# Performance work log

Hardware: AMD Instinct MI355X
Metric: run time of the kernel (lower is better)

The kernel has to match this reference:

```python
import jax, jax.numpy as jnp
import numpy as np

B, S, D = 2, 2048, 1024
E, K, F = 8, 2, 4 * D


def setup_inputs() -> dict:
    key = jax.random.key(0)
    ks = jax.random.split(key, 5)
    sd = 1.0 / np.sqrt(D)
    sf = 1.0 / np.sqrt(F)
    x = jax.random.normal(ks[0], (B, S, D), dtype=jnp.float32)
    Wg = jax.random.uniform(ks[1], (D, E), dtype=jnp.float32, minval=-sd, maxval=sd)
    W1 = jax.random.uniform(ks[2], (E, D, F), dtype=jnp.float32, minval=-sd, maxval=sd)
    W3 = jax.random.uniform(ks[3], (D, E * F), dtype=jnp.float32, minval=-sd, maxval=sd).reshape(D, E, F).transpose(1, 0, 2)
    W2 = jax.random.uniform(ks[4], (E, F, D), dtype=jnp.float32, minval=-sf, maxval=sf)
    return {"x": x, "Wg": Wg, "W1": W1, "W2": W2, "W3": W3}


def reference(x, Wg, W1, W2, W3):
    Bx, Sx, Dx = x.shape
    xf = x.reshape(-1, Dx)  # [T, D]
    T = xf.shape[0]
    gate_logits = xf @ Wg  # [T, E]
    probs = jax.nn.softmax(gate_logits, axis=-1)
    weights, sel = jax.lax.top_k(probs, K)  # [T, K]
    weights = weights / jnp.sum(weights, axis=-1, keepdims=True)
    # scatter top-k weights into a dense [T, E] combine matrix (top-k indices are distinct)
    coef = jnp.zeros((T, W1.shape[0]), dtype=xf.dtype)
    coef = coef.at[jnp.arange(T)[:, None], sel].add(weights)
    out = jnp.zeros_like(xf)
    for e in range(W1.shape[0]):  # small fixed expert count
        h = jax.nn.silu(xf @ W1[e]) * (xf @ W3[e])  # [T, F]
        out = out + coef[:, e:e + 1] * (h @ W2[e])
    aux_loss = jnp.mean(jnp.var(gate_logits, axis=-1, ddof=1))  # torch .var() is unbiased
    return out.reshape(Bx, Sx, Dx), aux_loss
```

## Files before the change

kernel.cpp:

```cpp
#include <hip/hip_runtime.h>

typedef __bf16 bf16x8 __attribute__((ext_vector_type(8)));
typedef float  f32x4  __attribute__((ext_vector_type(4)));

#define TOKS 4096
#define DIM  1024
#define NEXP 8
#define NF   4096
#define CAP  4096
#define BM 128
#define BN 128
#define BK 64

typedef __attribute__((address_space(3))) unsigned int as3_u32;
typedef __attribute__((address_space(1))) unsigned int as1_u32;
__device__ __forceinline__ void gl16(const unsigned short* g, unsigned short* l) {
  __builtin_amdgcn_global_load_lds((as1_u32*)(unsigned long long)g, (as3_u32*)l, 16, 0, 0);
}

__device__ __forceinline__ unsigned short f2bf(float f) {
  unsigned int u = __float_as_uint(f);
  u += 0x7FFFu + ((u >> 16) & 1u);
  return (unsigned short)(u >> 16);
}
__device__ __forceinline__ int swzo(int major) {
  return ((major & 7) ^ ((major >> 3) & 7)) << 3;
}
__device__ __forceinline__ int swz8(int row, int chunk) {
  return (chunk ^ (row & 7)) << 3;
}

__global__ void moe_route(const float* __restrict__ x, const float* __restrict__ Wg,
                          int* __restrict__ pairCnt, int* __restrict__ pairIdx,
                          float* __restrict__ pairWgt, float* __restrict__ auxSum)
{
  int lane = threadIdx.x & 63;
  int tok  = blockIdx.x * 4 + (threadIdx.x >> 6);
  const float* xr = x + (size_t)tok * DIM;
  float acc[8];
  #pragma unroll
  for (int e = 0; e < 8; ++e) acc[e] = 0.f;
  #pragma unroll
  for (int i = 0; i < 16; ++i) {
    int d = i * 64 + lane;
    float xv = xr[d];
    const float4* wr = (const float4*)(Wg + d * 8);
    float4 wa = wr[0], wb = wr[1];
    acc[0] += xv * wa.x; acc[1] += xv * wa.y; acc[2] += xv * wa.z; acc[3] += xv * wa.w;
    acc[4] += xv * wb.x; acc[5] += xv * wb.y; acc[6] += xv * wb.z; acc[7] += xv * wb.w;
  }
  #pragma unroll
  for (int e = 0; e < 8; ++e) {
    float v = acc[e];
    #pragma unroll
    for (int off = 32; off; off >>= 1) v += __shfl_xor(v, off);
    acc[e] = v;
  }
  if (lane == 0) {
    int e1 = 0; float l1 = acc[0];
    #pragma unroll
    for (int e = 1; e < 8; ++e) if (acc[e] > l1) { l1 = acc[e]; e1 = e; }
    int e2 = -1; float l2 = -3.4e38f;
    #pragma unroll
    for (int e = 0; e < 8; ++e) if (e != e1 && acc[e] > l2) { l2 = acc[e]; e2 = e; }
    float r  = expf(l2 - l1);
    float w1 = 1.f / (1.f + r);
    float w2 = r / (1.f + r);
    int s1 = atomicAdd(&pairCnt[e1], 1);
    pairIdx[e1 * CAP + s1] = tok * 2;     pairWgt[e1 * CAP + s1] = w1;
    int s2 = atomicAdd(&pairCnt[e2], 1);
    pairIdx[e2 * CAP + s2] = tok * 2 + 1; pairWgt[e2 * CAP + s2] = w2;
    float m = 0.f;
    #pragma unroll
    for (int e = 0; e < 8; ++e) m += acc[e];
    m *= 0.125f;
    float v = 0.f;
    #pragma unroll
    for (int e = 0; e < 8; ++e) { float dd = acc[e] - m; v += dd * dd; }
    atomicAdd(auxSum, v * (1.f / 7.f));
  }
}

__global__ void moe_aux_final(const float* __restrict__ auxSum, float* __restrict__ outScalar) {
  *outScalar = auxSum[0] * (1.f / (float)TOKS);
}

__global__ __launch_bounds__(256) void cvt_x(const float* __restrict__ in,
                                             unsigned short* __restrict__ o)
{
  int i = (blockIdx.x * 256 + threadIdx.x) * 16;
  const float4* s = (const float4*)(in + i);
  float4 a = s[0], b = s[1], c = s[2], d = s[3];
  union { unsigned short u[8]; uint4 q; } p0, p1;
  p0.u[0]=f2bf(a.x); p0.u[1]=f2bf(a.y); p0.u[2]=f2bf(a.z); p0.u[3]=f2bf(a.w);
  p0.u[4]=f2bf(b.x); p0.u[5]=f2bf(b.y); p0.u[6]=f2bf(b.z); p0.u[7]=f2bf(b.w);
  p1.u[0]=f2bf(c.x); p1.u[1]=f2bf(c.y); p1.u[2]=f2bf(c.z); p1.u[3]=f2bf(c.w);
  p1.u[4]=f2bf(d.x); p1.u[5]=f2bf(d.y); p1.u[6]=f2bf(d.z); p1.u[7]=f2bf(d.w);
  *(uint4*)(o + i)     = p0.q;
  *(uint4*)(o + i + 8) = p1.q;
}

__global__ __launch_bounds__(256) void cvt_transpose(
    const float* __restrict__ in, unsigned short* __restrict__ outp, int R, int C)
{
  __shared__ unsigned short tile[64 * 72];
  int e  = blockIdx.z;
  int r0 = blockIdx.x * 64, c0 = blockIdx.y * 64;
  const float*    ine  = in   + (size_t)e * R * C;
  unsigned short* oute = outp + (size_t)e * R * C;
  int t = threadIdx.x;
  int r = t >> 2, cs = (t & 3) * 16;
  const float4* src = (const float4*)(ine + (size_t)(r0 + r) * C + c0 + cs);
  #pragma unroll
  for (int j = 0; j < 4; ++j) {
    float4 v = src[j];
    tile[(cs + j * 4 + 0) * 72 + r] = f2bf(v.x);
    tile[(cs + j * 4 + 1) * 72 + r] = f2bf(v.y);
    tile[(cs + j * 4 + 2) * 72 + r] = f2bf(v.z);
    tile[(cs + j * 4 + 3) * 72 + r] = f2bf(v.w);
  }
  __syncthreads();
  int c = t >> 2, rs = (t & 3) * 16;
  uint4 o0 = *(const uint4*)&tile[c * 72 + rs];
  uint4 o1 = *(const uint4*)&tile[c * 72 + rs + 8];
  unsigned short* dst = oute + (size_t)(c0 + c) * R + r0 + rs;
  *(uint4*)dst       = o0;
  *(uint4*)(dst + 8) = o1;
}

__global__ __launch_bounds__(256) void cvt_w13(
    const float* __restrict__ W1, const float* __restrict__ W3,
    unsigned short* __restrict__ outp)
{
  __shared__ unsigned short t1[64 * 72];
  __shared__ unsigned short t3[64 * 72];
  int e  = blockIdx.z;
  int r0 = blockIdx.x * 64, c0 = blockIdx.y * 64;
  const float* in1 = W1 + (size_t)e * DIM * NF;
  const float* in3 = W3 + (size_t)e * DIM * NF;
  unsigned short* oute = outp + (size_t)e * (2 * NF) * DIM;
  int t = threadIdx.x;
  int r = t >> 2, cs = (t & 3) * 16;
  const float4* s1 = (const float4*)(in1 + (size_t)(r0 + r) * NF + c0 + cs);
  const float4* s3 = (const float4*)(in3 + (size_t)(r0 + r) * NF + c0 + cs);
  #pragma unroll
  for (int j = 0; j < 4; ++j) {
    float4 v1 = s1[j];
    float4 v3 = s3[j];
    int cb = cs + j * 4;
    t1[(cb + 0) * 72 + r] = f2bf(v1.x);
    t1[(cb + 1) * 72 + r] = f2bf(v1.y);
    t1[(cb + 2) * 72 + r] = f2bf(v1.z);
    t1[(cb + 3) * 72 + r] = f2bf(v1.w);
    t3[(cb + 0) * 72 + r] = f2bf(v3.x);
    t3[(cb + 1) * 72 + r] = f2bf(v3.y);
    t3[(cb + 2) * 72 + r] = f2bf(v3.z);
    t3[(cb + 3) * 72 + r] = f2bf(v3.w);
  }
  __syncthreads();
  int c = t >> 2, rs = (t & 3) * 16;
  int drow = c0 * 2 + (c >> 4) * 32 + (c & 15);
  uint4 a0 = *(const uint4*)&t1[c * 72 + rs];
  uint4 a1 = *(const uint4*)&t1[c * 72 + rs + 8];
  uint4 b0 = *(const uint4*)&t3[c * 72 + rs];
  uint4 b1 = *(const uint4*)&t3[c * 72 + rs + 8];
  unsigned short* d1 = oute + (size_t)drow * DIM + r0 + rs;
  unsigned short* d3 = d1 + (size_t)16 * DIM;
  *(uint4*)d1       = a0;
  *(uint4*)(d1 + 8) = a1;
  *(uint4*)d3       = b0;
  *(uint4*)(d3 + 8) = b1;
}

#define FFN1_PHASE(CUR, NXT, KS, Q, STG, DOWAIT, KTN) do {                       \
  int kc_ = (KS) * 4 + (lane >> 4);                                              \
  int sz_ = ((kc_ ^ (lane & 7)) << 3);                                           \
  int ar_ = wr * 128 + (Q) * 64 + (lane & 15);                                   \
  int br_ = wc * 64 + (lane & 15);                                               \
  bf16x8 a0_ = *(const bf16x8*)&As_[CUR][(ar_     ) * 64 + sz_];                 \
  bf16x8 a1_ = *(const bf16x8*)&As_[CUR][(ar_ + 16) * 64 + sz_];                 \
  bf16x8 a2_ = *(const bf16x8*)&As_[CUR][(ar_ + 32) * 64 + sz_];                 \
  bf16x8 a3_ = *(const bf16x8*)&As_[CUR][(ar_ + 48) * 64 + sz_];                 \
  bf16x8 b0_ = *(const bf16x8*)&Bs_[CUR][(br_     ) * 64 + sz_];                 \
  bf16x8 b1_ = *(const bf16x8*)&Bs_[CUR][(br_ + 16) * 64 + sz_];                 \
  bf16x8 b2_ = *(const bf16x8*)&Bs_[CUR][(br_ + 32) * 64 + sz_];                 \
  bf16x8 b3_ = *(const bf16x8*)&Bs_[CUR][(br_ + 48) * 64 + sz_];                 \
  if ((STG) == 1) {                                                              \
    gl16(pA[0][0] + (KTN), &As_[NXT][(w * 16      ) * 64]);                      \
    gl16(pA[0][1] + (KTN), &As_[NXT][(w * 16 +   8) * 64]);                      \
    gl16(pA[1][0] + (KTN), &As_[NXT][(w * 16 + 128) * 64]);                      \
    gl16(pA[1][1] + (KTN), &As_[NXT][(w * 16 + 136) * 64]);                      \
  } else if ((STG) == 2) {                                                       \
    gl16(pB[0][0] + (KTN), &Bs_[NXT][(w * 16      ) * 64]);                      \
    gl16(pB[0][1] + (KTN), &Bs_[NXT][(w * 16 +   8) * 64]);                      \
    gl16(pB[1][0] + (KTN), &Bs_[NXT][(w * 16 + 128) * 64]);                      \
    gl16(pB[1][1] + (KTN), &Bs_[NXT][(w * 16 + 136) * 64]);                      \
  }                                                                              \
  if (DOWAIT) {                                                                  \
    asm volatile("s_waitcnt lgkmcnt(0)" ::: "memory");                           \
    asm volatile("s_waitcnt vmcnt(0)" ::: "memory");                             \
  }                                                                              \
  __builtin_amdgcn_s_barrier();                                                  \
  __builtin_amdgcn_s_setprio(1);                                                 \
  acc[(Q)*4+0][0] = __builtin_amdgcn_mfma_f32_16x16x32_bf16(a0_, b0_, acc[(Q)*4+0][0], 0,0,0); \
  acc[(Q)*4+1][0] = __builtin_amdgcn_mfma_f32_16x16x32_bf16(a1_, b0_, acc[(Q)*4+1][0], 0,0,0); \
  acc[(Q)*4+2][0] = __builtin_amdgcn_mfma_f32_16x16x32_bf16(a2_, b0_, acc[(Q)*4+2][0], 0,0,0); \
  acc[(Q)*4+3][0] = __builtin_amdgcn_mfma_f32_16x16x32_bf16(a3_, b0_, acc[(Q)*4+3][0], 0,0,0); \
  acc[(Q)*4+0][1] = __builtin_amdgcn_mfma_f32_16x16x32_bf16(a0_, b1_, acc[(Q)*4+0][1], 0,0,0); \
  acc[(Q)*4+1][1] = __builtin_amdgcn_mfma_f32_16x16x32_bf16(a1_, b1_, acc[(Q)*4+1][1], 0,0,0); \
  acc[(Q)*4+2][1] = __builtin_amdgcn_mfma_f32_16x16x32_bf16(a2_, b1_, acc[(Q)*4+2][1], 0,0,0); \
  acc[(Q)*4+3][1] = __builtin_amdgcn_mfma_f32_16x16x32_bf16(a3_, b1_, acc[(Q)*4+3][1], 0,0,0); \
  acc[(Q)*4+0][2] = __builtin_amdgcn_mfma_f32_16x16x32_bf16(a0_, b2_, acc[(Q)*4+0][2], 0,0,0); \
  acc[(Q)*4+1][2] = __builtin_amdgcn_mfma_f32_16x16x32_bf16(a1_, b2_, acc[(Q)*4+1][2], 0,0,0); \
  acc[(Q)*4+2][2] = __builtin_amdgcn_mfma_f32_16x16x32_bf16(a2_, b2_, acc[(Q)*4+2][2], 0,0,0); \
  acc[(Q)*4+3][2] = __builtin_amdgcn_mfma_f32_16x16x32_bf16(a3_, b2_, acc[(Q)*4+3][2], 0,0,0); \
  acc[(Q)*4+0][3] = __builtin_amdgcn_mfma_f32_16x16x32_bf16(a0_, b3_, acc[(Q)*4+0][3], 0,0,0); \
  acc[(Q)*4+1][3] = __builtin_amdgcn_mfma_f32_16x16x32_bf16(a1_, b3_, acc[(Q)*4+1][3], 0,0,0); \
  acc[(Q)*4+2][3] = __builtin_amdgcn_mfma_f32_16x16x32_bf16(a2_, b3_, acc[(Q)*4+2][3], 0,0,0); \
  acc[(Q)*4+3][3] = __builtin_amdgcn_mfma_f32_16x16x32_bf16(a3_, b3_, acc[(Q)*4+3][3], 0,0,0); \
  __builtin_amdgcn_s_setprio(0);                                                 \
} while (0)

#define FFN1_GROUP(CUR, NXT, KTN)           \
  FFN1_PHASE(CUR, NXT, 0, 0, 1, 0, KTN);    \
  FFN1_PHASE(CUR, NXT, 0, 1, 2, 0, KTN);    \
  FFN1_PHASE(CUR, NXT, 1, 0, 0, 0, KTN);    \
  FFN1_PHASE(CUR, NXT, 1, 1, 0, 1, KTN);

__global__ __launch_bounds__(512, 2) void moe_ffn1_8p(
    const unsigned short* __restrict__ xbf, const unsigned short* __restrict__ W13T,
    const int* __restrict__ pairCnt, const int* __restrict__ pairIdx,
    unsigned short* __restrict__ hbuf)
{
  int bid = blockIdx.x;
  int n_t = (bid & 7) | (((bid >> 7) & 3) << 3);
  int m_t = (bid >> 3) & 15;
  int e   = bid >> 9;
  int cnt = pairCnt[e];
  int m0  = m_t * 256;
  if (m0 >= cnt) return;
  __shared__ __attribute__((aligned(16))) unsigned short As_[2][256 * 64];
  __shared__ __attribute__((aligned(16))) unsigned short Bs_[2][256 * 64];
  __shared__ int rowPid[256];
  int tid = threadIdx.x, lane = tid & 63, w = tid >> 6;
  if (tid < 256) {
    int gi = m0 + tid;
    rowPid[tid] = (gi < cnt) ? pairIdx[e * CAP + gi] : -1;
  }
  const unsigned short* W13e = W13T + (size_t)e * (2 * NF) * DIM + (size_t)n_t * 256 * DIM;
  int wr = w >> 2, wc = w & 3;
  f32x4 zero = {0.f, 0.f, 0.f, 0.f};
  f32x4 acc[8][4];
  #pragma unroll
  for (int mi = 0; mi < 8; ++mi)
    #pragma unroll
    for (int ni = 0; ni < 4; ++ni) acc[mi][ni] = zero;
  __syncthreads();

  int sr = w * 16 + (lane >> 3);
  int sc = ((lane & 7) ^ (lane >> 3)) * 8;
  const unsigned short* pA[2][2];
  const unsigned short* pB[2][2];
  #pragma unroll
  for (int h = 0; h < 2; ++h) {
    #pragma unroll
    for (int k = 0; k < 2; ++k) {
      int R = h * 128 + sr + k * 8;
      int pid = rowPid[R];
      pA[h][k] = xbf + (size_t)((pid >= 0) ? (pid >> 1) : 0) * DIM + sc;
      pB[h][k] = W13e + (size_t)R * DIM + sc;
    }
  }
  gl16(pA[0][0], &As_[0][(w * 16      ) * 64]);
  gl16(pA[0][1], &As_[0][(w * 16 +   8) * 64]);
  gl16(pA[1][0], &As_[0][(w * 16 + 128) * 64]);
  gl16(pA[1][1], &As_[0][(w * 16 + 136) * 64]);
  gl16(pB[0][0], &Bs_[0][(w * 16      ) * 64]);
  gl16(pB[0][1], &Bs_[0][(w * 16 +   8) * 64]);
  gl16(pB[1][0], &Bs_[0][(w * 16 + 128) * 64]);
  gl16(pB[1][1], &Bs_[0][(w * 16 + 136) * 64]);
  asm volatile("s_waitcnt vmcnt(0)" ::: "memory");
  __builtin_amdgcn_s_barrier();

  for (int j = 0; j < 16; j += 2) {
    int ktn0 = (j + 1) * 64;
    int ktn1 = (j + 2 < 16) ? (j + 2) * 64 : (j + 1) * 64;
    FFN1_GROUP(0, 1, ktn0);
    FFN1_GROUP(1, 0, ktn1);
  }

  #pragma unroll
  for (int mi = 0; mi < 8; ++mi) {
    #pragma unroll
    for (int r = 0; r < 4; ++r) {
      int row = wr * 128 + mi * 16 + ((lane >> 4) << 2) + r;
      int pid = rowPid[row];
      if (pid < 0) continue;
      size_t hb = (size_t)pid * NF + n_t * 128 + wc * 32 + (lane & 15);
      #pragma unroll
      for (int fg = 0; fg < 2; ++fg) {
        float a = acc[mi][fg * 2 + 0][r];
        float g = acc[mi][fg * 2 + 1][r];
        float s = 1.f / (1.f + __expf(-a));
        hbuf[hb + fg * 16] = f2bf(a * s * g);
      }
    }
  }
}

__global__ __launch_bounds__(512) void moe_ffn2_g(
    const unsigned short* __restrict__ hbuf, const unsigned short* __restrict__ W2T,
    const int* __restrict__ pairCnt, const int* __restrict__ pairIdx,
    const float* __restrict__ pairWgt, float* __restrict__ out)
{
  int bid = blockIdx.x;
  int n_t = bid & 7;
  int m_t = (bid >> 3) & 31;
  int e   = bid >> 8;
  int cnt = pairCnt[e];
  int m0  = m_t * BM;
  if (m0 >= cnt) return;
  int n0  = n_t * BN;
  __shared__ __attribute__((aligned(16))) unsigned short As[BM * BK];
  __shared__ __attribute__((aligned(16))) unsigned short Bs[BN * BK];
  __shared__ int   rowPid[BM];
  __shared__ float rowW[BM];
  int tid = threadIdx.x, lane = tid & 63, wid = tid >> 6;
  if (tid < BM) {
    int gi = m0 + tid;
    if (gi < cnt) { rowPid[tid] = pairIdx[e * CAP + gi]; rowW[tid] = pairWgt[e * CAP + gi]; }
    else          { rowPid[tid] = -1;                    rowW[tid] = 0.f; }
  }
  const unsigned short* W2e = W2T + (size_t)e * DIM * NF + (size_t)n0 * NF;
  f32x4 zero = {0.f, 0.f, 0.f, 0.f};
  f32x4 acc[2][4];
  #pragma unroll
  for (int mi = 0; mi < 2; ++mi)
    #pragma unroll
    for (int ni = 0; ni < 4; ++ni) acc[mi][ni] = zero;
  int wm = (wid >> 1) * 32, wn = (wid & 1) * 64;
  __syncthreads();

  int r0a = wid * 16 + (lane >> 3), r1a = r0a + 8;
  int p0 = rowPid[r0a], p1 = rowPid[r1a];
  size_t h0 = (size_t)((p0 >= 0) ? p0 : 0);
  size_t h1 = (size_t)((p1 >= 0) ? p1 : 0);
  int ch0 = ((lane & 7) ^ (r0a & 7)) * 8;
  int ch1 = ((lane & 7) ^ (r1a & 7)) * 8;
  const unsigned short* gA0 = hbuf + h0 * NF + ch0;
  const unsigned short* gA1 = hbuf + h1 * NF + ch1;
  const unsigned short* gB0 = W2e + (size_t)r0a * NF + ch0;
  const unsigned short* gB1 = W2e + (size_t)r1a * NF + ch1;
  unsigned short* lA0 = &As[(wid * 16) * BK];
  unsigned short* lA1 = &As[(wid * 16 + 8) * BK];
  unsigned short* lB0 = &Bs[(wid * 16) * BK];
  unsigned short* lB1 = &Bs[(wid * 16 + 8) * BK];

  for (int kt = 0; kt < NF; kt += BK) {
    gl16(gA0 + kt, lA0); gl16(gA1 + kt, lA1);
    gl16(gB0 + kt, lB0); gl16(gB1 + kt, lB1);
    __syncthreads();
    #pragma unroll
    for (int ks = 0; ks < 2; ++ks) {
      int kc = ks * 4 + (lane >> 4);
      bf16x8 af[2];
      #pragma unroll
      for (int mi = 0; mi < 2; ++mi) {
        int row = wm + mi * 16 + (lane & 15);
        af[mi] = *(const bf16x8*)(&As[row * BK + swz8(row, kc)]);
      }
      #pragma unroll
      for (int ni = 0; ni < 4; ++ni) {
        int dc = wn + ni * 16 + (lane & 15);
        bf16x8 b = *(const bf16x8*)(&Bs[dc * BK + swz8(dc, kc)]);
        #pragma unroll
        for (int mi = 0; mi < 2; ++mi)
          acc[mi][ni] = __builtin_amdgcn_mfma_f32_16x16x32_bf16(af[mi], b, acc[mi][ni], 0, 0, 0);
      }
    }
    __syncthreads();
  }
  #pragma unroll
  for (int mi = 0; mi < 2; ++mi) {
    #pragma unroll
    for (int r = 0; r < 4; ++r) {
      int row = wm + mi * 16 + ((lane >> 4) << 2) + r;
      int pid = rowPid[row];
      if (pid < 0) continue;
      float w = rowW[row];
      float* op = out + (size_t)(pid >> 1) * DIM + n0 + wn + (lane & 15);
      #pragma unroll
      for (int ni = 0; ni < 4; ++ni)
        atomicAdd(op + ni * 16, w * acc[mi][ni][r]);
    }
  }
}

__global__ __launch_bounds__(512) void moe_ffn1(
    const float* __restrict__ x, const float* __restrict__ W1, const float* __restrict__ W3,
    const int* __restrict__ pairCnt, const int* __restrict__ pairIdx,
    unsigned short* __restrict__ hbuf)
{
  int e   = blockIdx.z;
  int cnt = pairCnt[e];
  int m0  = blockIdx.x * BM;
  if (m0 >= cnt) return;
  int n0  = blockIdx.y * BN;
  __shared__ __attribute__((aligned(16))) unsigned short As[BM * BK];
  __shared__ __attribute__((aligned(16))) unsigned short B1s[BN * BK];
  __shared__ __attribute__((aligned(16))) unsigned short B3s[BN * BK];
  __shared__ int rowPid[BM];
  int tid = threadIdx.x;
  if (tid < BM) {
    int gi = m0 + tid;
    rowPid[tid] = (gi < cnt) ? pairIdx[e * CAP + gi] : -1;
  }
  const float* W1e = W1 + (size_t)e * DIM * NF;
  const float* W3e = W3 + (size_t)e * DIM * NF;
  f32x4 zero = {0.f, 0.f, 0.f, 0.f};
  f32x4 acc1[2][4], acc2[2][4];
  #pragma unroll
  for (int mi = 0; mi < 2; ++mi)
    #pragma unroll
    for (int ni = 0; ni < 4; ++ni) { acc1[mi][ni] = zero; acc2[mi][ni] = zero; }
  int lane = tid & 63, wid = tid >> 6;
  int wm = (wid >> 1) * 32, wn = (wid & 1) * 64;

  for (int kt = 0; kt < DIM; kt += BK) {
    __syncthreads();
    #pragma unroll
    for (int it = 0; it < 4; ++it) {
      int row = it * 32 + (tid >> 4);
      int dq  = tid & 15;
      int pid = rowPid[row];
      int tk  = (pid >= 0) ? (pid >> 1) : 0;
      float4 v = *(const float4*)(x + (size_t)tk * DIM + kt + dq * 4);
      ushort4 b; b.x = f2bf(v.x); b.y = f2bf(v.y); b.z = f2bf(v.z); b.w = f2bf(v.w);
      *(ushort4*)(&As[row * BK + ((dq * 4) ^ swzo(row))]) = b;
    }
    #pragma unroll
    for (int it = 0; it < 4; ++it) {
      int d  = it * 16 + (tid >> 5);
      int fq = tid & 31;
      size_t go = (size_t)(kt + d) * NF + n0 + fq * 4;
      float4 v1 = *(const float4*)(W1e + go);
      float4 v3 = *(const float4*)(W3e + go);
      const float* p1 = (const float*)&v1;
      const float* p3 = (const float*)&v3;
      #pragma unroll
      for (int i = 0; i < 4; ++i) {
        int f   = fq * 4 + i;
        int idx = f * BK + (d ^ swzo(f));
        B1s[idx] = f2bf(p1[i]);
        B3s[idx] = f2bf(p3[i]);
      }
    }
    __syncthreads();
    #pragma unroll
    for (int ks = 0; ks < 2; ++ks) {
      int kb = ks * 32 + ((lane >> 4) << 3);
      bf16x8 af[2];
      #pragma unroll
      for (int mi = 0; mi < 2; ++mi) {
        int row = wm + mi * 16 + (lane & 15);
        af[mi] = *(const bf16x8*)(&As[row * BK + (kb ^ swzo(row))]);
      }
      #pragma unroll
      for (int ni = 0; ni < 4; ++ni) {
        int f = wn + ni * 16 + (lane & 15);
        bf16x8 b1 = *(const bf16x8*)(&B1s[f * BK + (kb ^ swzo(f))]);
        bf16x8 b3 = *(const bf16x8*)(&B3s[f * BK + (kb ^ swzo(f))]);
        #pragma unroll
        for (int mi = 0; mi < 2; ++mi) {
          acc1[mi][ni] = __builtin_amdgcn_mfma_f32_16x16x32_bf16(af[mi], b1, acc1[mi][ni], 0, 0, 0);
          acc2[mi][ni] = __builtin_amdgcn_mfma_f32_16x16x32_bf16(af[mi], b3, acc2[mi][ni], 0, 0, 0);
        }
      }
    }
  }
  #pragma unroll
  for (int mi = 0; mi < 2; ++mi) {
    #pragma unroll
    for (int r = 0; r < 4; ++r) {
      int row = wm + mi * 16 + ((lane >> 4) << 2) + r;
      int pid = rowPid[row];
      if (pid < 0) continue;
      size_t hb = (size_t)pid * NF + n0 + wn + (lane & 15);
      #pragma unroll
      for (int ni = 0; ni < 4; ++ni) {
        float a = acc1[mi][ni][r];
        float g = acc2[mi][ni][r];
        float s = 1.f / (1.f + __expf(-a));
        hbuf[hb + ni * 16] = f2bf(a * s * g);
      }
    }
  }
}

__global__ __launch_bounds__(512) void moe_ffn2(
    const unsigned short* __restrict__ hbuf, const float* __restrict__ W2,
    const int* __restrict__ pairCnt, const int* __restrict__ pairIdx,
    const float* __restrict__ pairWgt, float* __restrict__ out)
{
  int e   = blockIdx.z;
  int cnt = pairCnt[e];
  int m0  = blockIdx.x * BM;
  if (m0 >= cnt) return;
  int n0  = blockIdx.y * BN;
  __shared__ __attribute__((aligned(16))) unsigned short As[BM * BK];
  __shared__ __attribute__((aligned(16))) unsigned short Bs[BN * BK];
  __shared__ int   rowPid[BM];
  __shared__ float rowW[BM];
  int tid = threadIdx.x;
  if (tid < BM) {
    int gi = m0 + tid;
    if (gi < cnt) { rowPid[tid] = pairIdx[e * CAP + gi]; rowW[tid] = pairWgt[e * CAP + gi]; }
    else          { rowPid[tid] = -1;                    rowW[tid] = 0.f; }
  }
  const float* W2e = W2 + (size_t)e * NF * DIM;
  f32x4 zero = {0.f, 0.f, 0.f, 0.f};
  f32x4 acc[2][4];
  #pragma unroll
  for (int mi = 0; mi < 2; ++mi)
    #pragma unroll
    for (int ni = 0; ni < 4; ++ni) acc[mi][ni] = zero;
  int lane = tid & 63, wid = tid >> 6;
  int wm = (wid >> 1) * 32, wn = (wid & 1) * 64;

  for (int kt = 0; kt < NF; kt += BK) {
    __syncthreads();
    #pragma unroll
    for (int it = 0; it < 2; ++it) {
      int row = it * 64 + (tid >> 3);
      int c8  = tid & 7;
      int pid = rowPid[row];
      int pr  = (pid >= 0) ? pid : 0;
      uint4 v = *(const uint4*)(hbuf + (size_t)pr * NF + kt + c8 * 8);
      *(uint4*)(&As[row * BK + ((c8 * 8) ^ swzo(row))]) = v;
    }
    #pragma unroll
    for (int it = 0; it < 4; ++it) {
      int fk = it * 16 + (tid >> 5);
      int dq = tid & 31;
      float4 v = *(const float4*)(W2e + (size_t)(kt + fk) * DIM + n0 + dq * 4);
      const float* p = (const float*)&v;
      #pragma unroll
      for (int i = 0; i < 4; ++i) {
        int dc = dq * 4 + i;
        Bs[dc * BK + (fk ^ swzo(dc))] = f2bf(p[i]);
      }
    }
    __syncthreads();
    #pragma unroll
    for (int ks = 0; ks < 2; ++ks) {
      int kb = ks * 32 + ((lane >> 4) << 3);
      bf16x8 af[2];
      #pragma unroll
      for (int mi = 0; mi < 2; ++mi) {
        int row = wm + mi * 16 + (lane & 15);
        af[mi] = *(const bf16x8*)(&As[row * BK + (kb ^ swzo(row))]);
      }
      #pragma unroll
      for (int ni = 0; ni < 4; ++ni) {
        int dc = wn + ni * 16 + (lane & 15);
        bf16x8 b = *(const bf16x8*)(&Bs[dc * BK + (kb ^ swzo(dc))]);
        #pragma unroll
        for (int mi = 0; mi < 2; ++mi)
          acc[mi][ni] = __builtin_amdgcn_mfma_f32_16x16x32_bf16(af[mi], b, acc[mi][ni], 0, 0, 0);
      }
    }
  }
  #pragma unroll
  for (int mi = 0; mi < 2; ++mi) {
    #pragma unroll
    for (int r = 0; r < 4; ++r) {
      int row = wm + mi * 16 + ((lane >> 4) << 2) + r;
      int pid = rowPid[row];
      if (pid < 0) continue;
      float w = rowW[row];
      float* op = out + (size_t)(pid >> 1) * DIM + n0 + wn + (lane & 15);
      #pragma unroll
      for (int ni = 0; ni < 4; ++ni)
        atomicAdd(op + ni * 16, w * acc[mi][ni][r]);
    }
  }
}

extern "C" void kernel_launch(void* const* d_in, const int* in_sizes, int n_in,
                              void* d_out, int out_size, void* d_ws, size_t ws_size,
                              hipStream_t stream)
{
  const float* x  = (const float*)d_in[0];
  const float* Wg = (const float*)d_in[1];
  const float* W1 = (const float*)d_in[2];
  const float* W2 = (const float*)d_in[3];
  const float* W3 = (const float*)d_in[4];
  float* out = (float*)d_out;
  char*  ws  = (char*)d_ws;
  int*   pairCnt = (int*)ws;
  float* auxSum  = (float*)(ws + 64);
  int*   pairIdx = (int*)(ws + 4096);
  float* pairWgt = (float*)(ws + 262144);
  unsigned short* xbf  = (unsigned short*)(ws + ((size_t)1 << 20));
  unsigned short* hbuf = (unsigned short*)(ws + ((size_t)9 << 20));
  unsigned short* W13T = (unsigned short*)(ws + ((size_t)73 << 20));
  unsigned short* W2T  = (unsigned short*)(ws + ((size_t)201 << 20));
  const size_t WS_NEED = (size_t)265 << 20;

  hipMemsetAsync(ws, 0, 128, stream);
  hipMemsetAsync(d_out, 0, (size_t)out_size * sizeof(float), stream);
  moe_route<<<TOKS / 4, 256, 0, stream>>>(x, Wg, pairCnt, pairIdx, pairWgt, auxSum);
  moe_aux_final<<<1, 1, 0, stream>>>(auxSum, out + (out_size - 1));

  if (ws_size >= WS_NEED) {
    cvt_x<<<TOKS * DIM / (256 * 16), 256, 0, stream>>>(x, xbf);
    cvt_w13<<<dim3(DIM / 64, NF / 64, NEXP), 256, 0, stream>>>(W1, W3, W13T);
    cvt_transpose<<<dim3(NF / 64, DIM / 64, NEXP), 256, 0, stream>>>(W2, W2T, NF, DIM);
    moe_ffn1_8p<<<16 * 32 * NEXP, 512, 0, stream>>>(xbf, W13T, pairCnt, pairIdx, hbuf);
    moe_ffn2_g<<<(TOKS / BM) * (DIM / BN) * NEXP, 512, 0, stream>>>(hbuf, W2T, pairCnt, pairIdx, pairWgt, out);
  } else {
    moe_ffn1<<<dim3(TOKS / BM, NF / BN, NEXP), 512, 0, stream>>>(x, W1, W3, pairCnt, pairIdx, hbuf);
    moe_ffn2<<<dim3(TOKS / BM, DIM / BN, NEXP), 512, 0, stream>>>(hbuf, W2, pairCnt, pairIdx, pairWgt, out);
  }
}
```

Baseline: 583.3 us.

## Restructure FFN1 into quadrant phases with split loads and partial vmcnt waits

Reworks the FFN1 GEMM main loop so each 256x256 tile is computed as four quadrant phases. Each wave handles a 64x32 sub-block per quadrant and covers the full BK=64 per phase. Global-to-LDS prefetch of the next tile is split into four two-load stages spread across the phases, with partial vmcnt waits instead of a full drain. The goal is smoother overlap of global loads with MFMA work. In exchange it adds an extra barrier per phase, changes the warp-to-output mapping and the epilogue indexing, and uses more live A/B fragments per phase.

```diff
diff --git a/kernel.cpp b/kernel.cpp
--- a/kernel.cpp
+++ b/kernel.cpp
@@ -172,60 +172,67 @@
   *(uint4*)(d3 + 8) = b1;
 }
 
-#define FFN1_PHASE(CUR, NXT, KS, Q, STG, DOWAIT, KTN) do {                       \
-  int kc_ = (KS) * 4 + (lane >> 4);                                              \
-  int sz_ = ((kc_ ^ (lane & 7)) << 3);                                           \
-  int ar_ = wr * 128 + (Q) * 64 + (lane & 15);                                   \
-  int br_ = wc * 64 + (lane & 15);                                               \
-  bf16x8 a0_ = *(const bf16x8*)&As_[CUR][(ar_     ) * 64 + sz_];                 \
-  bf16x8 a1_ = *(const bf16x8*)&As_[CUR][(ar_ + 16) * 64 + sz_];                 \
-  bf16x8 a2_ = *(const bf16x8*)&As_[CUR][(ar_ + 32) * 64 + sz_];                 \
-  bf16x8 a3_ = *(const bf16x8*)&As_[CUR][(ar_ + 48) * 64 + sz_];                 \
-  bf16x8 b0_ = *(const bf16x8*)&Bs_[CUR][(br_     ) * 64 + sz_];                 \
-  bf16x8 b1_ = *(const bf16x8*)&Bs_[CUR][(br_ + 16) * 64 + sz_];                 \
-  bf16x8 b2_ = *(const bf16x8*)&Bs_[CUR][(br_ + 32) * 64 + sz_];                 \
-  bf16x8 b3_ = *(const bf16x8*)&Bs_[CUR][(br_ + 48) * 64 + sz_];                 \
-  if ((STG) == 1) {                                                              \
-    gl16(pA[0][0] + (KTN), &As_[NXT][(w * 16      ) * 64]);                      \
-    gl16(pA[0][1] + (KTN), &As_[NXT][(w * 16 +   8) * 64]);                      \
-    gl16(pA[1][0] + (KTN), &As_[NXT][(w * 16 + 128) * 64]);                      \
-    gl16(pA[1][1] + (KTN), &As_[NXT][(w * 16 + 136) * 64]);                      \
+#define FFN1_PHASE(BUF, QM, QN, STG, VMC, KTN) do {                              \
+  int kl_  = lane >> 4;                                                          \
+  int szl_ = ((kl_ ^ (lane & 7)) << 3);                                          \
+  int szh_ = (((kl_ + 4) ^ (lane & 7)) << 3);                                    \
+  int ar_  = ((QM) * 128 + wr2 * 64 + (lane & 15)) * 64;                         \
+  int br_  = ((QN) * 128 + wc2 * 32 + (lane & 15)) * 64;                         \
+  bf16x8 aL0_ = *(const bf16x8*)&As_[BUF][ar_ +  0 * 64 + szl_];                 \
+  bf16x8 aL1_ = *(const bf16x8*)&As_[BUF][ar_ + 16 * 64 + szl_];                 \
+  bf16x8 aL2_ = *(const bf16x8*)&As_[BUF][ar_ + 32 * 64 + szl_];                 \
+  bf16x8 aL3_ = *(const bf16x8*)&As_[BUF][ar_ + 48 * 64 + szl_];                 \
+  bf16x8 aH0_ = *(const bf16x8*)&As_[BUF][ar_ +  0 * 64 + szh_];                 \
+  bf16x8 aH1_ = *(const bf16x8*)&As_[BUF][ar_ + 16 * 64 + szh_];                 \
+  bf16x8 aH2_ = *(const bf16x8*)&As_[BUF][ar_ + 32 * 64 + szh_];                 \
+  bf16x8 aH3_ = *(const bf16x8*)&As_[BUF][ar_ + 48 * 64 + szh_];                 \
+  bf16x8 bL0_ = *(const bf16x8*)&Bs_[BUF][br_ +  0 * 64 + szl_];                 \
+  bf16x8 bL1_ = *(const bf16x8*)&Bs_[BUF][br_ + 16 * 64 + szl_];                 \
+  bf16x8 bH0_ = *(const bf16x8*)&Bs_[BUF][br_ +  0 * 64 + szh_];                 \
+  bf16x8 bH1_ = *(const bf16x8*)&Bs_[BUF][br_ + 16 * 64 + szh_];                 \
+  if ((STG) == 0) {                                                              \
+    gl16(pA[0][0] + (KTN), &As_[(BUF)^1][(w * 16      ) * 64]);                  \
+    gl16(pA[0][1] + (KTN), &As_[(BUF)^1][(w * 16 +   8) * 64]);                  \
+  } else if ((STG) == 1) {                                                       \
+    gl16(pB[0][0] + (KTN), &Bs_[(BUF)^1][(w * 16      ) * 64]);                  \
+    gl16(pB[0][1] + (KTN), &Bs_[(BUF)^1][(w * 16 +   8) * 64]);                  \
   } else if ((STG) == 2) {                                                       \
-    gl16(pB[0][0] + (KTN), &Bs_[NXT][(w * 16      ) * 64]);                      \
-    gl16(pB[0][1] + (KTN), &Bs_[NXT][(w * 16 +   8) * 64]);                      \
-    gl16(pB[1][0] + (KTN), &Bs_[NXT][(w * 16 + 128) * 64]);                      \
-    gl16(pB[1][1] + (KTN), &Bs_[NXT][(w * 16 + 136) * 64]);                      \
+    gl16(pA[1][0] + (KTN), &As_[(BUF)^1][(w * 16 + 128) * 64]);                  \
+    gl16(pA[1][1] + (KTN), &As_[(BUF)^1][(w * 16 + 136) * 64]);                  \
+  } else {                                                                       \
+    gl16(pB[1][0] + (KTN), &Bs_[(BUF)^1][(w * 16 + 128) * 64]);                  \
+    gl16(pB[1][1] + (KTN), &Bs_[(BUF)^1][(w * 16 + 136) * 64]);                  \
   }                                                                              \
-  if (DOWAIT) {                                                                  \
-    asm volatile("s_waitcnt lgkmcnt(0)" ::: "memory");                           \
-    asm volatile("s_waitcnt vmcnt(0)" ::: "memory");                             \
-  }                                                                              \
+  if ((VMC) == 2) asm volatile("s_waitcnt vmcnt(2)" ::: "memory");               \
+  if ((VMC) == 4) asm volatile("s_waitcnt vmcnt(4)" ::: "memory");               \
   __builtin_amdgcn_s_barrier();                                                  \
+  asm volatile("s_waitcnt lgkmcnt(0)" ::: "memory");                             \
   __builtin_amdgcn_s_setprio(1);                                                 \
-  acc[(Q)*4+0][0] = __builtin_amdgcn_mfma_f32_16x16x32_bf16(a0_, b0_, acc[(Q)*4+0][0], 0,0,0); \
-  acc[(Q)*4+1][0] = __builtin_amdgcn_mfma_f32_16x16x32_bf16(a1_, b0_, acc[(Q)*4+1][0], 0,0,0); \
-  acc[(Q)*4+2][0] = __builtin_amdgcn_mfma_f32_16x16x32_bf16(a2_, b0_, acc[(Q)*4+2][0], 0,0,0); \
-  acc[(Q)*4+3][0] = __builtin_amdgcn_mfma_f32_16x16x32_bf16(a3_, b0_, acc[(Q)*4+3][0], 0,0,0); \
-  acc[(Q)*4+0][1] = __builtin_amdgcn_mfma_f32_16x16x32_bf16(a0_, b1_, acc[(Q)*4+0][1], 0,0,0); \
-  acc[(Q)*4+1][1] = __builtin_amdgcn_mfma_f32_16x16x32_bf16(a1_, b1_, acc[(Q)*4+1][1], 0,0,0); \
-  acc[(Q)*4+2][1] = __builtin_amdgcn_mfma_f32_16x16x32_bf16(a2_, b1_, acc[(Q)*4+2][1], 0,0,0); \
-  acc[(Q)*4+3][1] = __builtin_amdgcn_mfma_f32_16x16x32_bf16(a3_, b1_, acc[(Q)*4+3][1], 0,0,0); \
-  acc[(Q)*4+0][2] = __builtin_amdgcn_mfma_f32_16x16x32_bf16(a0_, b2_, acc[(Q)*4+0][2], 0,0,0); \
-  acc[(Q)*4+1][2] = __builtin_amdgcn_mfma_f32_16x16x32_bf16(a1_, b2_, acc[(Q)*4+1][2], 0,0,0); \
-  acc[(Q)*4+2][2] = __builtin_amdgcn_mfma_f32_16x16x32_bf16(a2_, b2_, acc[(Q)*4+2][2], 0,0,0); \
-  acc[(Q)*4+3][2] = __builtin_amdgcn_mfma_f32_16x16x32_bf16(a3_, b2_, acc[(Q)*4+3][2], 0,0,0); \
-  acc[(Q)*4+0][3] = __builtin_amdgcn_mfma_f32_16x16x32_bf16(a0_, b3_, acc[(Q)*4+0][3], 0,0,0); \
-  acc[(Q)*4+1][3] = __builtin_amdgcn_mfma_f32_16x16x32_bf16(a1_, b3_, acc[(Q)*4+1][3], 0,0,0); \
-  acc[(Q)*4+2][3] = __builtin_amdgcn_mfma_f32_16x16x32_bf16(a2_, b3_, acc[(Q)*4+2][3], 0,0,0); \
-  acc[(Q)*4+3][3] = __builtin_amdgcn_mfma_f32_16x16x32_bf16(a3_, b3_, acc[(Q)*4+3][3], 0,0,0); \
+  acc[(QM)*2+(QN)][0][0] = __builtin_amdgcn_mfma_f32_16x16x32_bf16(aL0_, bL0_, acc[(QM)*2+(QN)][0][0], 0,0,0); \
+  acc[(QM)*2+(QN)][1][0] = __builtin_amdgcn_mfma_f32_16x16x32_bf16(aL1_, bL0_, acc[(QM)*2+(QN)][1][0], 0,0,0); \
+  acc[(QM)*2+(QN)][2][0] = __builtin_amdgcn_mfma_f32_16x16x32_bf16(aL2_, bL0_, acc[(QM)*2+(QN)][2][0], 0,0,0); \
+  acc[(QM)*2+(QN)][3][0] = __builtin_amdgcn_mfma_f32_16x16x32_bf16(aL3_, bL0_, acc[(QM)*2+(QN)][3][0], 0,0,0); \
+  acc[(QM)*2+(QN)][0][1] = __builtin_amdgcn_mfma_f32_16x16x32_bf16(aL0_, bL1_, acc[(QM)*2+(QN)][0][1], 0,0,0); \
+  acc[(QM)*2+(QN)][1][1] = __builtin_amdgcn_mfma_f32_16x16x32_bf16(aL1_, bL1_, acc[(QM)*2+(QN)][1][1], 0,0,0); \
+  acc[(QM)*2+(QN)][2][1] = __builtin_amdgcn_mfma_f32_16x16x32_bf16(aL2_, bL1_, acc[(QM)*2+(QN)][2][1], 0,0,0); \
+  acc[(QM)*2+(QN)][3][1] = __builtin_amdgcn_mfma_f32_16x16x32_bf16(aL3_, bL1_, acc[(QM)*2+(QN)][3][1], 0,0,0); \
+  acc[(QM)*2+(QN)][0][0] = __builtin_amdgcn_mfma_f32_16x16x32_bf16(aH0_, bH0_, acc[(QM)*2+(QN)][0][0], 0,0,0); \
+  acc[(QM)*2+(QN)][1][0] = __builtin_amdgcn_mfma_f32_16x16x32_bf16(aH1_, bH0_, acc[(QM)*2+(QN)][1][0], 0,0,0); \
+  acc[(QM)*2+(QN)][2][0] = __builtin_amdgcn_mfma_f32_16x16x32_bf16(aH2_, bH0_, acc[(QM)*2+(QN)][2][0], 0,0,0); \
+  acc[(QM)*2+(QN)][3][0] = __builtin_amdgcn_mfma_f32_16x16x32_bf16(aH3_, bH0_, acc[(QM)*2+(QN)][3][0], 0,0,0); \
+  acc[(QM)*2+(QN)][0][1] = __builtin_amdgcn_mfma_f32_16x16x32_bf16(aH0_, bH1_, acc[(QM)*2+(QN)][0][1], 0,0,0); \
+  acc[(QM)*2+(QN)][1][1] = __builtin_amdgcn_mfma_f32_16x16x32_bf16(aH1_, bH1_, acc[(QM)*2+(QN)][1][1], 0,0,0); \
+  acc[(QM)*2+(QN)][2][1] = __builtin_amdgcn_mfma_f32_16x16x32_bf16(aH2_, bH1_, acc[(QM)*2+(QN)][2][1], 0,0,0); \
+  acc[(QM)*2+(QN)][3][1] = __builtin_amdgcn_mfma_f32_16x16x32_bf16(aH3_, bH1_, acc[(QM)*2+(QN)][3][1], 0,0,0); \
   __builtin_amdgcn_s_setprio(0);                                                 \
+  __builtin_amdgcn_s_barrier();                                                  \
 } while (0)
 
-#define FFN1_GROUP(CUR, NXT, KTN)           \
-  FFN1_PHASE(CUR, NXT, 0, 0, 1, 0, KTN);    \
-  FFN1_PHASE(CUR, NXT, 0, 1, 2, 0, KTN);    \
-  FFN1_PHASE(CUR, NXT, 1, 0, 0, 0, KTN);    \
-  FFN1_PHASE(CUR, NXT, 1, 1, 0, 1, KTN);
+#define FFN1_TILE(BUF, KTN)               \
+  FFN1_PHASE(BUF, 0, 0, 0,  2, KTN);      \
+  FFN1_PHASE(BUF, 0, 1, 1, -1, KTN);      \
+  FFN1_PHASE(BUF, 1, 0, 2, -1, KTN);      \
+  FFN1_PHASE(BUF, 1, 1, 3,  4, KTN);
 
 __global__ __launch_bounds__(512, 2) void moe_ffn1_8p(
     const unsigned short* __restrict__ xbf, const unsigned short* __restrict__ W13T,
@@ -248,13 +255,15 @@
     rowPid[tid] = (gi < cnt) ? pairIdx[e * CAP + gi] : -1;
   }
   const unsigned short* W13e = W13T + (size_t)e * (2 * NF) * DIM + (size_t)n_t * 256 * DIM;
-  int wr = w >> 2, wc = w & 3;
+  int wr2 = w >> 2, wc2 = w & 3;
   f32x4 zero = {0.f, 0.f, 0.f, 0.f};
-  f32x4 acc[8][4];
-  #pragma unroll
-  for (int mi = 0; mi < 8; ++mi)
-    #pragma unroll
-    for (int ni = 0; ni < 4; ++ni) acc[mi][ni] = zero;
+  f32x4 acc[4][4][2];
+  #pragma unroll
+  for (int q = 0; q < 4; ++q)
+    #pragma unroll
+    for (int mi = 0; mi < 4; ++mi)
+      #pragma unroll
+      for (int ni = 0; ni < 2; ++ni) acc[q][mi][ni] = zero;
   __syncthreads();
 
   int sr = w * 16 + (lane >> 3);
@@ -273,36 +282,37 @@
   }
   gl16(pA[0][0], &As_[0][(w * 16      ) * 64]);
   gl16(pA[0][1], &As_[0][(w * 16 +   8) * 64]);
+  gl16(pB[0][0], &Bs_[0][(w * 16      ) * 64]);
+  gl16(pB[0][1], &Bs_[0][(w * 16 +   8) * 64]);
   gl16(pA[1][0], &As_[0][(w * 16 + 128) * 64]);
   gl16(pA[1][1], &As_[0][(w * 16 + 136) * 64]);
-  gl16(pB[0][0], &Bs_[0][(w * 16      ) * 64]);
-  gl16(pB[0][1], &Bs_[0][(w * 16 +   8) * 64]);
   gl16(pB[1][0], &Bs_[0][(w * 16 + 128) * 64]);
   gl16(pB[1][1], &Bs_[0][(w * 16 + 136) * 64]);
-  asm volatile("s_waitcnt vmcnt(0)" ::: "memory");
+  asm volatile("s_waitcnt vmcnt(4)" ::: "memory");
   __builtin_amdgcn_s_barrier();
 
   for (int j = 0; j < 16; j += 2) {
     int ktn0 = (j + 1) * 64;
-    int ktn1 = (j + 2 < 16) ? (j + 2) * 64 : (j + 1) * 64;
-    FFN1_GROUP(0, 1, ktn0);
-    FFN1_GROUP(1, 0, ktn1);
-  }
-
-  #pragma unroll
-  for (int mi = 0; mi < 8; ++mi) {
-    #pragma unroll
-    for (int r = 0; r < 4; ++r) {
-      int row = wr * 128 + mi * 16 + ((lane >> 4) << 2) + r;
-      int pid = rowPid[row];
-      if (pid < 0) continue;
-      size_t hb = (size_t)pid * NF + n_t * 128 + wc * 32 + (lane & 15);
-      #pragma unroll
-      for (int fg = 0; fg < 2; ++fg) {
-        float a = acc[mi][fg * 2 + 0][r];
-        float g = acc[mi][fg * 2 + 1][r];
+    int ktn1 = (j + 2 < 16) ? (j + 2) * 64 : 15 * 64;
+    FFN1_TILE(0, ktn0);
+    FFN1_TILE(1, ktn1);
+  }
+
+  #pragma unroll
+  for (int q = 0; q < 4; ++q) {
+    int qm = q >> 1, qn = q & 1;
+    #pragma unroll
+    for (int mi = 0; mi < 4; ++mi) {
+      #pragma unroll
+      for (int r = 0; r < 4; ++r) {
+        int row = qm * 128 + wr2 * 64 + mi * 16 + ((lane >> 4) << 2) + r;
+        int pid = rowPid[row];
+        if (pid < 0) continue;
+        float a = acc[q][mi][0][r];
+        float g = acc[q][mi][1][r];
         float s = 1.f / (1.f + __expf(-a));
-        hbuf[hb + fg * 16] = f2bf(a * s * g);
+        size_t f = (size_t)n_t * 128 + (qn * 4 + wc2) * 16 + (lane & 15);
+        hbuf[(size_t)pid * NF + f] = f2bf(a * s * g);
       }
     }
   }
```

Measured after the change: 644.6 us. +10.5%, slower.
